# Performance work log

Measured on AMD Instinct MI355X. Metric: run time of the kernel, lower is better.

Reference implementation:

```python
import jax, jax.numpy as jnp
import numpy as np
from jax import lax


def _gather_xq(x_flat, qx, qy, w):
    # x_flat: [B, C, H*W]; qx, qy: [B, H, W] int32 -> [B, C, H, W]
    b, c, _ = x_flat.shape
    h, ww = qx.shape[1], qx.shape[2]
    idx = (qx * w + qy).reshape(b, 1, h * ww)  # [B,1,H*W]
    out = jnp.take_along_axis(x_flat, jnp.broadcast_to(idx, (b, c, h * ww)), axis=2)
    return out.reshape(b, c, h, ww)


def setup_inputs() -> dict:
    key = jax.random.key(0)
    k1, k2 = jax.random.split(key)
    B, C, H, W = 8, 256, 128, 128
    x = jax.random.normal(k1, (B, C, H, W), dtype=jnp.float32)
    w_conv = jax.random.normal(k2, (2, C, 3, 3), dtype=jnp.float32) * 0.02
    b_conv = jnp.zeros((2,), dtype=jnp.float32)
    return {"x": x, "w_conv": w_conv, "b_conv": b_conv}


def reference(x, w_conv, b_conv):
    B, C, H, W = x.shape
    # offset conv: Conv2d(inc, 2, k=3, stride=1, padding=1)
    offset = lax.conv_general_dilated(
        x, w_conv, window_strides=(1, 1), padding=((1, 1), (1, 1)),
        dimension_numbers=("NCHW", "OIHW", "NCHW"),
    ) + b_conv[None, :, None, None]  # [B, 2, H, W], N = 1

    # base grid p_0 (ij indexing as in torch.meshgrid legacy)
    p0_x = jnp.arange(H, dtype=x.dtype)[:, None] * jnp.ones((1, W), dtype=x.dtype)
    p0_y = jnp.ones((H, 1), dtype=x.dtype) * jnp.arange(W, dtype=x.dtype)[None, :]
    px = p0_x[None] + offset[:, 0]  # [B, H, W]
    py = p0_y[None] + offset[:, 1]

    px = jnp.clip(px, 0.0, H - 2)
    py = jnp.clip(py, 0.0, W - 2)

    # corner indices (detached in original via requires_grad=False)
    fx = lax.stop_gradient(jnp.floor(px))
    fy = lax.stop_gradient(jnp.floor(py))
    qx0 = fx.astype(jnp.int32)
    qy0 = fy.astype(jnp.int32)
    qx1 = qx0 + 1
    qy1 = qy0 + 1

    # bilinear weights
    g_lt = (1.0 + (fx - px)) * (1.0 + (fy - py))
    g_rb = (1.0 - (fx + 1.0 - px)) * (1.0 - (fy + 1.0 - py))
    g_lb = (1.0 + (fx - px)) * (1.0 - (fy + 1.0 - py))
    g_rt = (1.0 - (fx + 1.0 - px)) * (1.0 + (fy - py))

    x_flat = x.reshape(B, C, H * W)
    x_lt = _gather_xq(x_flat, qx0, qy0, W)
    x_rb = _gather_xq(x_flat, qx1, qy1, W)
    x_lb = _gather_xq(x_flat, qx0, qy1, W)
    x_rt = _gather_xq(x_flat, qx1, qy0, W)

    out = (g_lt[:, None] * x_lt + g_rb[:, None] * x_rb
           + g_lb[:, None] * x_lb + g_rt[:, None] * x_rt)  # [B, C, H, W]
    # original returns x_up_reset.squeeze(1): with C>1 and N=1 this keeps
    # the trailing sampling-point dim -> [B, C, H, W, 1]
    return out[..., None]
```

## Files before the change

kernel.cpp:

```cpp
#include <hip/hip_runtime.h>

#define Bn 8
#define Cn 256
#define Hn 128
#define Wn 128
#define HW (Hn * Wn)
#define NPIX (Bn * Hn * Wn)
#define NPAIR (NPIX / 2)

typedef float v2f  __attribute__((ext_vector_type(2)));
typedef float v2fu __attribute__((ext_vector_type(2), aligned(4)));
typedef float v4f  __attribute__((ext_vector_type(4)));

template <int CCH>
__global__ __launch_bounds__(256, 8) void conv_partial_kernel(
    const float* __restrict__ x, const float* __restrict__ wconv,
    float2* __restrict__ part)
{
    constexpr int CPC = Cn / CCH;
    const int pg    = blockIdx.x & 127;
    const int chunk = blockIdx.x >> 7;
    const int pq = pg * 256 + (int)threadIdx.x;
    const int lane = (int)threadIdx.x & 63;
    const int w0 = (pq & 31) << 2;
    const int h  = (pq >> 5) & (Hn - 1);
    const int b  = pq >> 12;

    const float* xb = x + ((size_t)(b * Cn + chunk * CPC)) * HW + h * Wn + w0;

    const bool hm = (h > 0), hp = (h < Hn - 1);
    const bool wm = (w0 > 0), wp = (w0 < Wn - 4);

    float a00 = 0.f, a01 = 0.f, a02 = 0.f, a03 = 0.f;
    float a10 = 0.f, a11 = 0.f, a12 = 0.f, a13 = 0.f;

    const float* w0b = wconv + chunk * CPC * 9;
    const float* w1b = wconv + Cn * 9 + chunk * CPC * 9;

    #pragma unroll 2
    for (int c = 0; c < CPC; ++c) {
        const float* xc = xb + c * HW;
        const float4 z4 = make_float4(0.f, 0.f, 0.f, 0.f);
        float4 m0 = hm ? *(const float4*)(xc - Wn) : z4;
        float4 m1 =      *(const float4*)(xc);
        float4 m2 = hp ? *(const float4*)(xc + Wn) : z4;

        float l0 = __shfl(m0.w, lane - 1), r0 = __shfl(m0.x, lane + 1);
        float l1 = __shfl(m1.w, lane - 1), r1 = __shfl(m1.x, lane + 1);
        float l2 = __shfl(m2.w, lane - 1), r2 = __shfl(m2.x, lane + 1);

        float v[3][6];
        v[0][0] = wm ? l0 : 0.f; v[0][1] = m0.x; v[0][2] = m0.y;
        v[0][3] = m0.z; v[0][4] = m0.w; v[0][5] = wp ? r0 : 0.f;
        v[1][0] = wm ? l1 : 0.f; v[1][1] = m1.x; v[1][2] = m1.y;
        v[1][3] = m1.z; v[1][4] = m1.w; v[1][5] = wp ? r1 : 0.f;
        v[2][0] = wm ? l2 : 0.f; v[2][1] = m2.x; v[2][2] = m2.y;
        v[2][3] = m2.z; v[2][4] = m2.w; v[2][5] = wp ? r2 : 0.f;

        const float* w0c = w0b + c * 9;
        const float* w1c = w1b + c * 9;
        #pragma unroll
        for (int r = 0; r < 3; ++r) {
            const float k0 = w0c[r*3+0], k1 = w0c[r*3+1], k2 = w0c[r*3+2];
            const float u0 = w1c[r*3+0], u1 = w1c[r*3+1], u2 = w1c[r*3+2];
            a00 = fmaf(v[r][0], k0, a00); a00 = fmaf(v[r][1], k1, a00); a00 = fmaf(v[r][2], k2, a00);
            a01 = fmaf(v[r][1], k0, a01); a01 = fmaf(v[r][2], k1, a01); a01 = fmaf(v[r][3], k2, a01);
            a02 = fmaf(v[r][2], k0, a02); a02 = fmaf(v[r][3], k1, a02); a02 = fmaf(v[r][4], k2, a02);
            a03 = fmaf(v[r][3], k0, a03); a03 = fmaf(v[r][4], k1, a03); a03 = fmaf(v[r][5], k2, a03);
            a10 = fmaf(v[r][0], u0, a10); a10 = fmaf(v[r][1], u1, a10); a10 = fmaf(v[r][2], u2, a10);
            a11 = fmaf(v[r][1], u0, a11); a11 = fmaf(v[r][2], u1, a11); a11 = fmaf(v[r][3], u2, a11);
            a12 = fmaf(v[r][2], u0, a12); a12 = fmaf(v[r][3], u1, a12); a12 = fmaf(v[r][4], u2, a12);
            a13 = fmaf(v[r][3], u0, a13); a13 = fmaf(v[r][4], u1, a13); a13 = fmaf(v[r][5], u2, a13);
        }
    }

    v4f* pt = (v4f*)(part + (size_t)chunk * NPIX + ((size_t)pq << 2));
    v4f s0 = {a00, a10, a01, a11};
    v4f s1 = {a02, a12, a03, a13};
    pt[0] = s0;
    pt[1] = s1;
}

template <int CCH>
__global__ __launch_bounds__(256, 8) void reduce_kernel(
    float2* __restrict__ part, const float* __restrict__ bconv)
{
    const int pp = blockIdx.x * 256 + (int)threadIdx.x;
    v4f* p4 = (v4f*)part;
    v4f q = p4[pp];
    #pragma unroll
    for (int k = 1; k < CCH; ++k) q += p4[(size_t)k * NPAIR + pp];

    const int pr  = pp & (HW / 2 - 1);
    const int hw0 = pr << 1;
    const int w = hw0 & (Wn - 1);
    const int h = hw0 >> 7;

    const float bc0 = bconv[0], bc1 = bconv[1];
    float px0 = (float)h + q.x + bc0;
    float py0 = (float)w + q.y + bc1;
    float px1 = (float)h + q.z + bc0;
    float py1 = (float)(w + 1) + q.w + bc1;
    px0 = fminf(fmaxf(px0, 0.f), (float)(Hn - 2));
    py0 = fminf(fmaxf(py0, 0.f), (float)(Wn - 2));
    px1 = fminf(fmaxf(px1, 0.f), (float)(Hn - 2));
    py1 = fminf(fmaxf(py1, 0.f), (float)(Wn - 2));

    v4f o = {px0, py0, px1, py1};
    p4[pp] = o;
}

#define SCH 8
#define SPC (Cn / SCH)

__global__ __launch_bounds__(256, 8) void sample_kernel(
    const float* __restrict__ x, const float2* __restrict__ part,
    float* __restrict__ out)
{
    const int tid = blockIdx.x * 256 + (int)threadIdx.x;
    const int pp    = tid & (NPAIR - 1);
    const int chunk = tid >> 16;
    const int pr  = pp & (HW / 2 - 1);
    const int b   = pp >> 13;
    const int hw0 = pr << 1;

    const v4f q = ((const v4f*)part)[pp];

    const float fx0 = floorf(q.x), fy0 = floorf(q.y);
    const float fx1 = floorf(q.z), fy1 = floorf(q.w);
    const float dx0 = q.x - fx0, dy0 = q.y - fy0;
    const float dx1 = q.z - fx1, dy1 = q.w - fy1;
    const int bs0 = (int)fx0 * Wn + (int)fy0;
    const int bs1 = (int)fx1 * Wn + (int)fy1;

    const float glt0 = (1.f - dx0) * (1.f - dy0), grb0 = dx0 * dy0;
    const float glb0 = (1.f - dx0) * dy0,         grt0 = dx0 * (1.f - dy0);
    const float glt1 = (1.f - dx1) * (1.f - dy1), grb1 = dx1 * dy1;
    const float glb1 = (1.f - dx1) * dy1,         grt1 = dx1 * (1.f - dy1);

    const size_t cb = ((size_t)(b * Cn + chunk * SPC)) * HW;
    const float* xb = x + cb;
    float* ob = out + cb + hw0;

    #pragma unroll 8
    for (int c = 0; c < SPC; ++c) {
        const float* xc = xb + (size_t)c * HW;
        v2fu A0 = *(const v2fu*)(xc + bs0);
        v2fu B0 = *(const v2fu*)(xc + bs0 + Wn);
        v2fu A1 = *(const v2fu*)(xc + bs1);
        v2fu B1 = *(const v2fu*)(xc + bs1 + Wn);
        const float o0 = glt0 * A0.x + glb0 * A0.y + grt0 * B0.x + grb0 * B0.y;
        const float o1 = glt1 * A1.x + glb1 * A1.y + grt1 * B1.x + grb1 * B1.y;
        v2f o = {o0, o1};
        __builtin_nontemporal_store(o, (v2f*)(ob + (size_t)c * HW));
    }
}

extern "C" void kernel_launch(void* const* d_in, const int* in_sizes, int n_in,
                              void* d_out, int out_size, void* d_ws, size_t ws_size,
                              hipStream_t stream) {
    const float* x     = (const float*)d_in[0];
    const float* wconv = (const float*)d_in[1];
    const float* bconv = (const float*)d_in[2];
    float* out = (float*)d_out;

    float2* part = (float2*)d_ws;

    if (ws_size >= (size_t)16 * NPIX * sizeof(float2)) {
        conv_partial_kernel<16><<<128 * 16, 256, 0, stream>>>(x, wconv, part);
        reduce_kernel<16><<<NPAIR / 256, 256, 0, stream>>>(part, bconv);
    } else if (ws_size >= (size_t)8 * NPIX * sizeof(float2)) {
        conv_partial_kernel<8><<<128 * 8, 256, 0, stream>>>(x, wconv, part);
        reduce_kernel<8><<<NPAIR / 256, 256, 0, stream>>>(part, bconv);
    } else {
        conv_partial_kernel<4><<<128 * 4, 256, 0, stream>>>(x, wconv, part);
        reduce_kernel<4><<<NPAIR / 256, 256, 0, stream>>>(part, bconv);
    }
    sample_kernel<<<(NPAIR * SCH) / 256, 256, 0, stream>>>(x, part, out);
}
```

Baseline: 313.4 us.

## Split each conv chunk across four wavefronts with shared-memory reduction

```diff
diff --git a/kernel.cpp b/kernel.cpp
--- a/kernel.cpp
+++ b/kernel.cpp
@@ -11,6 +11,78 @@
 typedef float v2f  __attribute__((ext_vector_type(2)));
 typedef float v2fu __attribute__((ext_vector_type(2), aligned(4)));
 typedef float v4f  __attribute__((ext_vector_type(4)));
+
+__global__ __launch_bounds__(256, 8) void conv_block_kernel(
+    const float* __restrict__ x, const float* __restrict__ wconv,
+    float2* __restrict__ part)
+{
+    __shared__ float red[8][4][64];
+    const int pg    = blockIdx.x & 511;
+    const int chunk = blockIdx.x >> 9;
+    const int q = (int)threadIdx.x >> 6;
+    const int l = (int)threadIdx.x & 63;
+    const int pq = pg * 64 + l;
+    const int w0 = (pq & 31) << 2;
+    const int h  = (pq >> 5) & (Hn - 1);
+    const int b  = pq >> 12;
+    const int c0 = chunk * 16 + q * 4;
+
+    const float* xb = x + ((size_t)(b * Cn + c0)) * HW + h * Wn + w0;
+
+    const bool hm = (h > 0), hp = (h < Hn - 1);
+    const bool wm = (w0 > 0), wp = (w0 < Wn - 4);
+
+    float a00 = 0.f, a01 = 0.f, a02 = 0.f, a03 = 0.f;
+    float a10 = 0.f, a11 = 0.f, a12 = 0.f, a13 = 0.f;
+
+    #pragma unroll
+    for (int i = 0; i < 4; ++i) {
+        const float* xc = xb + i * HW;
+        const float4 z4 = make_float4(0.f, 0.f, 0.f, 0.f);
+        float4 m0 = hm ? *(const float4*)(xc - Wn) : z4;
+        float4 m1 =      *(const float4*)(xc);
+        float4 m2 = hp ? *(const float4*)(xc + Wn) : z4;
+
+        float l0 = __shfl(m0.w, l - 1), r0 = __shfl(m0.x, l + 1);
+        float l1 = __shfl(m1.w, l - 1), r1 = __shfl(m1.x, l + 1);
+        float l2 = __shfl(m2.w, l - 1), r2 = __shfl(m2.x, l + 1);
+
+        float v[3][6];
+        v[0][0] = wm ? l0 : 0.f; v[0][1] = m0.x; v[0][2] = m0.y;
+        v[0][3] = m0.z; v[0][4] = m0.w; v[0][5] = wp ? r0 : 0.f;
+        v[1][0] = wm ? l1 : 0.f; v[1][1] = m1.x; v[1][2] = m1.y;
+        v[1][3] = m1.z; v[1][4] = m1.w; v[1][5] = wp ? r1 : 0.f;
+        v[2][0] = wm ? l2 : 0.f; v[2][1] = m2.x; v[2][2] = m2.y;
+        v[2][3] = m2.z; v[2][4] = m2.w; v[2][5] = wp ? r2 : 0.f;
+
+        const float* w0c = wconv + (c0 + i) * 9;
+        const float* w1c = wconv + Cn * 9 + (c0 + i) * 9;
+        #pragma unroll
+        for (int r = 0; r < 3; ++r) {
+            const float k0 = w0c[r*3+0], k1 = w0c[r*3+1], k2 = w0c[r*3+2];
+            const float u0 = w1c[r*3+0], u1 = w1c[r*3+1], u2 = w1c[r*3+2];
+            a00 = fmaf(v[r][0], k0, a00); a00 = fmaf(v[r][1], k1, a00); a00 = fmaf(v[r][2], k2, a00);
+            a01 = fmaf(v[r][1], k0, a01); a01 = fmaf(v[r][2], k1, a01); a01 = fmaf(v[r][3], k2, a01);
+            a02 = fmaf(v[r][2], k0, a02); a02 = fmaf(v[r][3], k1, a02); a02 = fmaf(v[r][4], k2, a02);
+            a03 = fmaf(v[r][3], k0, a03); a03 = fmaf(v[r][4], k1, a03); a03 = fmaf(v[r][5], k2, a03);
+            a10 = fmaf(v[r][0], u0, a10); a10 = fmaf(v[r][1], u1, a10); a10 = fmaf(v[r][2], u2, a10);
+            a11 = fmaf(v[r][1], u0, a11); a11 = fmaf(v[r][2], u1, a11); a11 = fmaf(v[r][3], u2, a11);
+            a12 = fmaf(v[r][2], u0, a12); a12 = fmaf(v[r][3], u1, a12); a12 = fmaf(v[r][4], u2, a12);
+            a13 = fmaf(v[r][3], u0, a13); a13 = fmaf(v[r][4], u1, a13); a13 = fmaf(v[r][5], u2, a13);
+        }
+    }
+
+    red[0][q][l] = a00; red[1][q][l] = a10;
+    red[2][q][l] = a01; red[3][q][l] = a11;
+    red[4][q][l] = a02; red[5][q][l] = a12;
+    red[6][q][l] = a03; red[7][q][l] = a13;
+    __syncthreads();
+
+    const int j0 = q << 1;
+    float s0 = red[j0][0][l] + red[j0][1][l] + red[j0][2][l] + red[j0][3][l];
+    float s1 = red[j0+1][0][l] + red[j0+1][1][l] + red[j0+1][2][l] + red[j0+1][3][l];
+    part[(size_t)chunk * NPIX + ((size_t)pq << 2) + q] = make_float2(s0, s1);
+}
 
 template <int CCH>
 __global__ __launch_bounds__(256, 8) void conv_partial_kernel(
@@ -167,7 +239,7 @@
     float2* part = (float2*)d_ws;
 
     if (ws_size >= (size_t)16 * NPIX * sizeof(float2)) {
-        conv_partial_kernel<16><<<128 * 16, 256, 0, stream>>>(x, wconv, part);
+        conv_block_kernel<<<512 * 16, 256, 0, stream>>>(x, wconv, part);
         reduce_kernel<16><<<NPAIR / 256, 256, 0, stream>>>(part, bconv);
     } else if (ws_size >= (size_t)8 * NPIX * sizeof(float2)) {
         conv_partial_kernel<8><<<128 * 8, 256, 0, stream>>>(x, wconv, part);
```

After: 637.9 us. 2.04x slower.
